# Kernel optimization log

Measured on AMD Instinct MI355X. Metric: run time of the kernel, lower is better.

## Reference

```python
import jax, jax.numpy as jnp
import numpy as np


def setup_inputs() -> dict:
    key = jax.random.key(0)
    k1, k2, k3 = jax.random.split(key, 3)
    B, S, K, N = 4, 2048, 4096, 4096
    x = jax.random.normal(k1, (B, S, K), dtype=jnp.float32)
    # int8 weight table, symmetric range like post-quantization weights
    weight = jax.random.randint(k2, (N, K), -127, 128, dtype=jnp.int32).astype(jnp.int8)
    weight_scale = jnp.float32(0.01)
    bias = jax.random.normal(k3, (N,), dtype=jnp.float32)
    return {"x": x, "weight": weight, "weight_scale": weight_scale, "bias": bias}


def reference(x, weight, weight_scale, bias):
    # dynamic per-tensor activation quantization
    input_scale = jnp.max(jnp.abs(x)) / 127.0
    # torch float->int8 cast truncates toward zero; XLA convert does the same
    x_int8 = jnp.clip(x / input_scale, -127.0, 127.0).astype(jnp.int8)
    orig_shape = x.shape
    # int8 GEMM with int32 accumulation (torch._int_mm equivalent)
    out_int32 = jnp.matmul(
        x_int8.reshape(-1, orig_shape[-1]), weight.T,
        preferred_element_type=jnp.int32,
    )
    out = out_int32.astype(x.dtype) * (input_scale * weight_scale)
    out = out.reshape(*orig_shape[:-1], weight.shape[0])
    out = out + bias
    return out
```

## Files before the change

### kernel.cpp

```cpp
#include <hip/hip_runtime.h>
#include <stdint.h>

static constexpr int KD = 4096;
static constexpr int ND = 4096;

using i32x4 = __attribute__((ext_vector_type(4))) int;

__device__ __forceinline__ void async_copy16(const void* g, void* l) {
    __builtin_amdgcn_global_load_lds(
        (const __attribute__((address_space(1))) void*)g,
        (__attribute__((address_space(3))) void*)l,
        16, 0, 0);
}

__global__ __launch_bounds__(256) void absmax_kernel(
        const float* __restrict__ x, unsigned* __restrict__ out_bits, int n4) {
    int tid = blockIdx.x * blockDim.x + threadIdx.x;
    int stride = gridDim.x * blockDim.x;
    const float4* x4 = (const float4*)x;
    float m = 0.f;
    for (int i = tid; i < n4; i += stride) {
        float4 v = x4[i];
        m = fmaxf(m, fmaxf(fmaxf(fabsf(v.x), fabsf(v.y)),
                           fmaxf(fabsf(v.z), fabsf(v.w))));
    }
    #pragma unroll
    for (int off = 32; off > 0; off >>= 1)
        m = fmaxf(m, __shfl_down(m, off, 64));
    __shared__ float wmax[4];
    int lane = threadIdx.x & 63, w = threadIdx.x >> 6;
    if (lane == 0) wmax[w] = m;
    __syncthreads();
    if (threadIdx.x == 0) {
        float b = fmaxf(fmaxf(wmax[0], wmax[1]), fmaxf(wmax[2], wmax[3]));
        atomicMax(out_bits, __float_as_uint(b));
    }
}

__global__ __launch_bounds__(256) void quant_x_kernel(
        const float* __restrict__ x, const unsigned* __restrict__ mx_bits,
        int8_t* __restrict__ xq) {
    int tid = blockIdx.x * blockDim.x + threadIdx.x;
    float s = __uint_as_float(*mx_bits) * (1.0f / 127.0f);
    const float4* x4 = (const float4*)(x + (size_t)tid * 16);
    int4 packed;
    int* pp = (int*)&packed;
    #pragma unroll
    for (int g = 0; g < 4; ++g) {
        float4 v = x4[g];
        float t0 = fminf(127.f, fmaxf(-127.f, v.x / s));
        float t1 = fminf(127.f, fmaxf(-127.f, v.y / s));
        float t2 = fminf(127.f, fmaxf(-127.f, v.z / s));
        float t3 = fminf(127.f, fmaxf(-127.f, v.w / s));
        int q0 = (int)t0, q1 = (int)t1, q2 = (int)t2, q3 = (int)t3;
        pp[g] = (q0 & 255) | ((q1 & 255) << 8) | ((q2 & 255) << 16) | (q3 << 24);
    }
    ((int4*)xq)[tid] = packed;
}

__global__ __launch_bounds__(256) void pack_w_kernel(
        const int* __restrict__ w, int8_t* __restrict__ wq) {
    int tid = blockIdx.x * blockDim.x + threadIdx.x;
    const int4* w4 = (const int4*)(w + (size_t)tid * 16);
    int4 packed;
    int* pp = (int*)&packed;
    #pragma unroll
    for (int g = 0; g < 4; ++g) {
        int4 v = w4[g];
        pp[g] = (v.x & 255) | ((v.y & 255) << 8) | ((v.z & 255) << 16) | (v.w << 24);
    }
    ((int4*)wq)[tid] = packed;
}

__global__ __launch_bounds__(256) void gemm_i8_kernel(
        const int8_t* __restrict__ Aq,
        const int8_t* __restrict__ Wq,
        const unsigned* __restrict__ mx_bits,
        const float* __restrict__ wscale_p,
        const float* __restrict__ bias,
        float* __restrict__ out) {
    __shared__ __align__(16) int8_t lds_a[128 * 64];
    __shared__ __align__(16) int8_t lds_b[128 * 64];

    const int bx = blockIdx.x;
    const int by = blockIdx.y;
    const int tid  = threadIdx.x;
    const int lane = tid & 63;
    const int w    = tid >> 6;
    const int wm = (w >> 1) * 64;
    const int wn = (w & 1) * 64;
    const int fr = lane & 15;
    const int kc = lane >> 4;

    const int r1 = tid >> 2;
    const int c1 = (tid & 3) ^ ((tid >> 3) & 3);
    const int r2 = r1 + 64;
    const size_t Abase = (size_t)by * 128 * KD;
    const size_t Bbase = (size_t)bx * 128 * KD;
    int8_t* ldsA1 = lds_a + (tid & 192) * 16;
    int8_t* ldsA2 = lds_a + 4096 + (tid & 192) * 16;
    int8_t* ldsB1 = lds_b + (tid & 192) * 16;
    int8_t* ldsB2 = lds_b + 4096 + (tid & 192) * 16;

    i32x4 acc[4][4] = {};

    for (int kt = 0; kt < KD / 64; ++kt) {
        const int k0 = kt * 64;
        async_copy16(Aq + Abase + (size_t)r1 * KD + k0 + c1 * 16, ldsA1);
        async_copy16(Aq + Abase + (size_t)r2 * KD + k0 + c1 * 16, ldsA2);
        async_copy16(Wq + Bbase + (size_t)r1 * KD + k0 + c1 * 16, ldsB1);
        async_copy16(Wq + Bbase + (size_t)r2 * KD + k0 + c1 * 16, ldsB2);
        __syncthreads();

        i32x4 af[4], bf[4];
        #pragma unroll
        for (int i = 0; i < 4; ++i) {
            int row = wm + i * 16 + fr;
            af[i] = *(const i32x4*)(lds_a + row * 64 +
                                    ((kc ^ ((row >> 1) & 3)) << 4));
        }
        #pragma unroll
        for (int j = 0; j < 4; ++j) {
            int row = wn + j * 16 + fr;
            bf[j] = *(const i32x4*)(lds_b + row * 64 +
                                    ((kc ^ ((row >> 1) & 3)) << 4));
        }
        #pragma unroll
        for (int i = 0; i < 4; ++i)
            #pragma unroll
            for (int j = 0; j < 4; ++j)
                acc[i][j] = __builtin_amdgcn_mfma_i32_16x16x64_i8(
                    af[i], bf[j], acc[i][j], 0, 0, 0);
        __syncthreads();
    }

    const float in_scale = __uint_as_float(*mx_bits) * (1.0f / 127.0f);
    const float stot = in_scale * (*wscale_p);
    float bj[4];
    #pragma unroll
    for (int j = 0; j < 4; ++j)
        bj[j] = bias[bx * 128 + wn + j * 16 + fr];

    #pragma unroll
    for (int i = 0; i < 4; ++i) {
        int mrow = by * 128 + wm + i * 16 + kc * 4;
        #pragma unroll
        for (int r = 0; r < 4; ++r) {
            float* orow = out + (size_t)(mrow + r) * ND + bx * 128;
            #pragma unroll
            for (int j = 0; j < 4; ++j)
                orow[wn + j * 16 + fr] = (float)acc[i][j][r] * stot + bj[j];
        }
    }
}

extern "C" void kernel_launch(void* const* d_in, const int* in_sizes, int n_in,
                              void* d_out, int out_size, void* d_ws, size_t ws_size,
                              hipStream_t stream) {
    const float* x      = (const float*)d_in[0];
    const int*   wgt    = (const int*)d_in[1];
    const float* wscale = (const float*)d_in[2];
    const float* bias   = (const float*)d_in[3];
    float* out = (float*)d_out;

    const int M = in_sizes[0] / KD;

    uint8_t* ws = (uint8_t*)d_ws;
    unsigned* mx_bits = (unsigned*)ws;
    int8_t* xq = (int8_t*)(ws + 256);
    int8_t* wq = (int8_t*)(ws + 256 + (size_t)M * KD);

    hipMemsetAsync(mx_bits, 0, 4, stream);
    absmax_kernel<<<1024, 256, 0, stream>>>(x, mx_bits, (M * KD) / 4);
    quant_x_kernel<<<(M * KD / 16) / 256, 256, 0, stream>>>(x, mx_bits, xq);
    pack_w_kernel<<<(ND * KD / 16) / 256, 256, 0, stream>>>(wgt, wq);
    gemm_i8_kernel<<<dim3(ND / 128, M / 128), 256, 0, stream>>>(
        xq, wq, mx_bits, wscale, bias, out);
}
```

Baseline: 451.1 us.

## Switch GEMM to 32x32x32 int8 MFMA and rework preprocessing kernels

The GEMM inner loop now uses 32x32x32 int8 MFMA instructions with 2x2 accumulators per wave instead of 4x4 tiles of 16x16x64, which cuts the instruction count and changes the LDS fragment loads and epilogue layout. The absmax kernel unrolls four independent loads per iteration and launches twice as many blocks. The quantize and pack kernels now handle 4 elements per thread instead of 16, using more threads with narrower stores. The scale is computed by division instead of multiplication by a reciprocal, which may change rounding slightly. The narrower 4-byte stores in the preprocessing kernels could reduce store efficiency.

```diff
diff --git a/kernel.cpp b/kernel.cpp
--- a/kernel.cpp
+++ b/kernel.cpp
@@ -4,7 +4,8 @@
 static constexpr int KD = 4096;
 static constexpr int ND = 4096;
 
-using i32x4 = __attribute__((ext_vector_type(4))) int;
+using i32x4  = __attribute__((ext_vector_type(4)))  int;
+using i32x16 = __attribute__((ext_vector_type(16))) int;
 
 __device__ __forceinline__ void async_copy16(const void* g, void* l) {
     __builtin_amdgcn_global_load_lds(
@@ -18,12 +19,22 @@
     int tid = blockIdx.x * blockDim.x + threadIdx.x;
     int stride = gridDim.x * blockDim.x;
     const float4* x4 = (const float4*)x;
-    float m = 0.f;
-    for (int i = tid; i < n4; i += stride) {
-        float4 v = x4[i];
-        m = fmaxf(m, fmaxf(fmaxf(fabsf(v.x), fabsf(v.y)),
-                           fmaxf(fabsf(v.z), fabsf(v.w))));
+    float m0 = 0.f, m1 = 0.f, m2 = 0.f, m3 = 0.f;
+    for (int i = tid; i < n4; i += 4 * stride) {
+        float4 a = x4[i];
+        float4 b = x4[i + stride];
+        float4 c = x4[i + 2 * stride];
+        float4 d = x4[i + 3 * stride];
+        m0 = fmaxf(m0, fmaxf(fmaxf(fabsf(a.x), fabsf(a.y)),
+                             fmaxf(fabsf(a.z), fabsf(a.w))));
+        m1 = fmaxf(m1, fmaxf(fmaxf(fabsf(b.x), fabsf(b.y)),
+                             fmaxf(fabsf(b.z), fabsf(b.w))));
+        m2 = fmaxf(m2, fmaxf(fmaxf(fabsf(c.x), fabsf(c.y)),
+                             fmaxf(fabsf(c.z), fabsf(c.w))));
+        m3 = fmaxf(m3, fmaxf(fmaxf(fabsf(d.x), fabsf(d.y)),
+                             fmaxf(fabsf(d.z), fabsf(d.w))));
     }
+    float m = fmaxf(fmaxf(m0, m1), fmaxf(m2, m3));
     #pragma unroll
     for (int off = 32; off > 0; off >>= 1)
         m = fmaxf(m, __shfl_down(m, off, 64));
@@ -41,35 +52,21 @@
         const float* __restrict__ x, const unsigned* __restrict__ mx_bits,
         int8_t* __restrict__ xq) {
     int tid = blockIdx.x * blockDim.x + threadIdx.x;
-    float s = __uint_as_float(*mx_bits) * (1.0f / 127.0f);
-    const float4* x4 = (const float4*)(x + (size_t)tid * 16);
-    int4 packed;
-    int* pp = (int*)&packed;
-    #pragma unroll
-    for (int g = 0; g < 4; ++g) {
-        float4 v = x4[g];
-        float t0 = fminf(127.f, fmaxf(-127.f, v.x / s));
-        float t1 = fminf(127.f, fmaxf(-127.f, v.y / s));
-        float t2 = fminf(127.f, fmaxf(-127.f, v.z / s));
-        float t3 = fminf(127.f, fmaxf(-127.f, v.w / s));
-        int q0 = (int)t0, q1 = (int)t1, q2 = (int)t2, q3 = (int)t3;
-        pp[g] = (q0 & 255) | ((q1 & 255) << 8) | ((q2 & 255) << 16) | (q3 << 24);
-    }
-    ((int4*)xq)[tid] = packed;
+    float s = __uint_as_float(*mx_bits) / 127.0f;
+    float4 v = ((const float4*)x)[tid];
+    float t0 = fminf(127.f, fmaxf(-127.f, v.x / s));
+    float t1 = fminf(127.f, fmaxf(-127.f, v.y / s));
+    float t2 = fminf(127.f, fmaxf(-127.f, v.z / s));
+    float t3 = fminf(127.f, fmaxf(-127.f, v.w / s));
+    int q0 = (int)t0, q1 = (int)t1, q2 = (int)t2, q3 = (int)t3;
+    ((int*)xq)[tid] = (q0 & 255) | ((q1 & 255) << 8) | ((q2 & 255) << 16) | (q3 << 24);
 }
 
 __global__ __launch_bounds__(256) void pack_w_kernel(
         const int* __restrict__ w, int8_t* __restrict__ wq) {
     int tid = blockIdx.x * blockDim.x + threadIdx.x;
-    const int4* w4 = (const int4*)(w + (size_t)tid * 16);
-    int4 packed;
-    int* pp = (int*)&packed;
-    #pragma unroll
-    for (int g = 0; g < 4; ++g) {
-        int4 v = w4[g];
-        pp[g] = (v.x & 255) | ((v.y & 255) << 8) | ((v.z & 255) << 16) | (v.w << 24);
-    }
-    ((int4*)wq)[tid] = packed;
+    int4 v = ((const int4*)w)[tid];
+    ((int*)wq)[tid] = (v.x & 255) | ((v.y & 255) << 8) | ((v.z & 255) << 16) | (v.w << 24);
 }
 
 __global__ __launch_bounds__(256) void gemm_i8_kernel(
@@ -89,8 +86,8 @@
     const int w    = tid >> 6;
     const int wm = (w >> 1) * 64;
     const int wn = (w & 1) * 64;
-    const int fr = lane & 15;
-    const int kc = lane >> 4;
+    const int r32 = lane & 31;
+    const int kh  = lane >> 5;
 
     const int r1 = tid >> 2;
     const int c1 = (tid & 3) ^ ((tid >> 3) & 3);
@@ -102,7 +99,7 @@
     int8_t* ldsB1 = lds_b + (tid & 192) * 16;
     int8_t* ldsB2 = lds_b + 4096 + (tid & 192) * 16;
 
-    i32x4 acc[4][4] = {};
+    i32x16 acc[2][2] = {};
 
     for (int kt = 0; kt < KD / 64; ++kt) {
         const int k0 = kt * 64;
@@ -112,44 +109,53 @@
         async_copy16(Wq + Bbase + (size_t)r2 * KD + k0 + c1 * 16, ldsB2);
         __syncthreads();
 
-        i32x4 af[4], bf[4];
+        i32x4 af[2][2], bf[2][2];
         #pragma unroll
-        for (int i = 0; i < 4; ++i) {
-            int row = wm + i * 16 + fr;
-            af[i] = *(const i32x4*)(lds_a + row * 64 +
-                                    ((kc ^ ((row >> 1) & 3)) << 4));
+        for (int i = 0; i < 2; ++i) {
+            int row = wm + i * 32 + r32;
+            int sw = (row >> 1) & 3;
+            #pragma unroll
+            for (int kk = 0; kk < 2; ++kk)
+                af[kk][i] = *(const i32x4*)(lds_a + row * 64 +
+                                            (((kk * 2 + kh) ^ sw) << 4));
         }
         #pragma unroll
-        for (int j = 0; j < 4; ++j) {
-            int row = wn + j * 16 + fr;
-            bf[j] = *(const i32x4*)(lds_b + row * 64 +
-                                    ((kc ^ ((row >> 1) & 3)) << 4));
+        for (int j = 0; j < 2; ++j) {
+            int row = wn + j * 32 + r32;
+            int sw = (row >> 1) & 3;
+            #pragma unroll
+            for (int kk = 0; kk < 2; ++kk)
+                bf[kk][j] = *(const i32x4*)(lds_b + row * 64 +
+                                            (((kk * 2 + kh) ^ sw) << 4));
         }
         #pragma unroll
-        for (int i = 0; i < 4; ++i)
+        for (int kk = 0; kk < 2; ++kk)
             #pragma unroll
-            for (int j = 0; j < 4; ++j)
-                acc[i][j] = __builtin_amdgcn_mfma_i32_16x16x64_i8(
-                    af[i], bf[j], acc[i][j], 0, 0, 0);
+            for (int i = 0; i < 2; ++i)
+                #pragma unroll
+                for (int j = 0; j < 2; ++j)
+                    acc[i][j] = __builtin_amdgcn_mfma_i32_32x32x32_i8(
+                        af[kk][i], bf[kk][j], acc[i][j], 0, 0, 0);
         __syncthreads();
     }
 
-    const float in_scale = __uint_as_float(*mx_bits) * (1.0f / 127.0f);
-    const float stot = in_scale * (*wscale_p);
-    float bj[4];
+    const float stot = (__uint_as_float(*mx_bits) / 127.0f) * (*wscale_p);
+    const int rquad = (lane >> 5) * 4;
+    float bj[2];
     #pragma unroll
-    for (int j = 0; j < 4; ++j)
-        bj[j] = bias[bx * 128 + wn + j * 16 + fr];
+    for (int j = 0; j < 2; ++j)
+        bj[j] = bias[bx * 128 + wn + j * 32 + r32];
 
     #pragma unroll
-    for (int i = 0; i < 4; ++i) {
-        int mrow = by * 128 + wm + i * 16 + kc * 4;
+    for (int i = 0; i < 2; ++i) {
         #pragma unroll
-        for (int r = 0; r < 4; ++r) {
-            float* orow = out + (size_t)(mrow + r) * ND + bx * 128;
+        for (int reg = 0; reg < 16; ++reg) {
+            int row_in = (reg & 3) + 8 * (reg >> 2) + rquad;
+            float* orow = out + (size_t)(by * 128 + wm + i * 32 + row_in) * ND
+                              + bx * 128;
             #pragma unroll
-            for (int j = 0; j < 4; ++j)
-                orow[wn + j * 16 + fr] = (float)acc[i][j][r] * stot + bj[j];
+            for (int j = 0; j < 2; ++j)
+                orow[wn + j * 32 + r32] = (float)acc[i][j][reg] * stot + bj[j];
         }
     }
 }
@@ -171,9 +177,9 @@
     int8_t* wq = (int8_t*)(ws + 256 + (size_t)M * KD);
 
     hipMemsetAsync(mx_bits, 0, 4, stream);
-    absmax_kernel<<<1024, 256, 0, stream>>>(x, mx_bits, (M * KD) / 4);
-    quant_x_kernel<<<(M * KD / 16) / 256, 256, 0, stream>>>(x, mx_bits, xq);
-    pack_w_kernel<<<(ND * KD / 16) / 256, 256, 0, stream>>>(wgt, wq);
+    absmax_kernel<<<2048, 256, 0, stream>>>(x, mx_bits, (M * KD) / 4);
+    quant_x_kernel<<<(M * KD / 4) / 256, 256, 0, stream>>>(x, mx_bits, xq);
+    pack_w_kernel<<<(ND * KD / 4) / 256, 256, 0, stream>>>(wgt, wq);
     gemm_i8_kernel<<<dim3(ND / 128, M / 128), 256, 0, stream>>>(
         xq, wq, mx_bits, wscale, bias, out);
 }
```

Measured after the change: 463.2 us. 2.7% more time.

## Fuse absmax with weight packing, widen GEMM K-tile, simplify quantization

Applied to the files above, without the earlier changes.

Merges the absmax reduction and the int8 weight packing into one prologue launch, with the reduction unrolled four ways for more loads in flight. The GEMM K tile grows from 64 to 128 bytes with an 8-way XOR swizzle, halving the number of barrier-separated iterations and doubling LDS use per block. The quantization kernel now handles one float4 per thread, and the scale is computed with an exact division by 127 to better match the reference. The larger LDS footprint may reduce occupancy, and the prologue's absmax loop assumes the element count divides evenly by four times the stride.

```diff
diff --git a/kernel.cpp b/kernel.cpp
--- a/kernel.cpp
+++ b/kernel.cpp
@@ -3,6 +3,7 @@
 
 static constexpr int KD = 4096;
 static constexpr int ND = 4096;
+static constexpr int BKB = 128;
 
 using i32x4 = __attribute__((ext_vector_type(4))) int;
 
@@ -13,27 +14,54 @@
         16, 0, 0);
 }
 
-__global__ __launch_bounds__(256) void absmax_kernel(
-        const float* __restrict__ x, unsigned* __restrict__ out_bits, int n4) {
-    int tid = blockIdx.x * blockDim.x + threadIdx.x;
-    int stride = gridDim.x * blockDim.x;
-    const float4* x4 = (const float4*)x;
-    float m = 0.f;
-    for (int i = tid; i < n4; i += stride) {
-        float4 v = x4[i];
-        m = fmaxf(m, fmaxf(fmaxf(fabsf(v.x), fabsf(v.y)),
-                           fmaxf(fabsf(v.z), fabsf(v.w))));
-    }
-    #pragma unroll
-    for (int off = 32; off > 0; off >>= 1)
-        m = fmaxf(m, __shfl_down(m, off, 64));
-    __shared__ float wmax[4];
-    int lane = threadIdx.x & 63, w = threadIdx.x >> 6;
-    if (lane == 0) wmax[w] = m;
-    __syncthreads();
-    if (threadIdx.x == 0) {
-        float b = fmaxf(fmaxf(wmax[0], wmax[1]), fmaxf(wmax[2], wmax[3]));
-        atomicMax(out_bits, __float_as_uint(b));
+static constexpr int AB_BLOCKS = 2048;
+
+__global__ __launch_bounds__(256) void prologue_kernel(
+        const float* __restrict__ x, unsigned* __restrict__ out_bits, int n4,
+        const int* __restrict__ w, int8_t* __restrict__ wq) {
+    if (blockIdx.x < AB_BLOCKS) {
+        int tid = blockIdx.x * blockDim.x + threadIdx.x;
+        int stride = AB_BLOCKS * 256;
+        const float4* x4 = (const float4*)x;
+        float m0 = 0.f, m1 = 0.f, m2 = 0.f, m3 = 0.f;
+        for (int i = tid; i < n4; i += 4 * stride) {
+            float4 a = x4[i];
+            float4 b = x4[i + stride];
+            float4 c = x4[i + 2 * stride];
+            float4 d = x4[i + 3 * stride];
+            m0 = fmaxf(m0, fmaxf(fmaxf(fabsf(a.x), fabsf(a.y)),
+                                 fmaxf(fabsf(a.z), fabsf(a.w))));
+            m1 = fmaxf(m1, fmaxf(fmaxf(fabsf(b.x), fabsf(b.y)),
+                                 fmaxf(fabsf(b.z), fabsf(b.w))));
+            m2 = fmaxf(m2, fmaxf(fmaxf(fabsf(c.x), fabsf(c.y)),
+                                 fmaxf(fabsf(c.z), fabsf(c.w))));
+            m3 = fmaxf(m3, fmaxf(fmaxf(fabsf(d.x), fabsf(d.y)),
+                                 fmaxf(fabsf(d.z), fabsf(d.w))));
+        }
+        float m = fmaxf(fmaxf(m0, m1), fmaxf(m2, m3));
+        #pragma unroll
+        for (int off = 32; off > 0; off >>= 1)
+            m = fmaxf(m, __shfl_down(m, off, 64));
+        __shared__ float wmax[4];
+        int lane = threadIdx.x & 63, wv = threadIdx.x >> 6;
+        if (lane == 0) wmax[wv] = m;
+        __syncthreads();
+        if (threadIdx.x == 0) {
+            float b = fmaxf(fmaxf(wmax[0], wmax[1]), fmaxf(wmax[2], wmax[3]));
+            atomicMax(out_bits, __float_as_uint(b));
+        }
+    } else {
+        int t = (blockIdx.x - AB_BLOCKS) * 256 + threadIdx.x;
+        const int4* w4 = (const int4*)(w) + (size_t)t * 4;
+        int4 packed;
+        int* pp = (int*)&packed;
+        #pragma unroll
+        for (int g = 0; g < 4; ++g) {
+            int4 v = w4[g];
+            pp[g] = (v.x & 255) | ((v.y & 255) << 8) |
+                    ((v.z & 255) << 16) | (v.w << 24);
+        }
+        ((int4*)wq)[t] = packed;
     }
 }
 
@@ -41,35 +69,15 @@
         const float* __restrict__ x, const unsigned* __restrict__ mx_bits,
         int8_t* __restrict__ xq) {
     int tid = blockIdx.x * blockDim.x + threadIdx.x;
-    float s = __uint_as_float(*mx_bits) * (1.0f / 127.0f);
-    const float4* x4 = (const float4*)(x + (size_t)tid * 16);
-    int4 packed;
-    int* pp = (int*)&packed;
-    #pragma unroll
-    for (int g = 0; g < 4; ++g) {
-        float4 v = x4[g];
-        float t0 = fminf(127.f, fmaxf(-127.f, v.x / s));
-        float t1 = fminf(127.f, fmaxf(-127.f, v.y / s));
-        float t2 = fminf(127.f, fmaxf(-127.f, v.z / s));
-        float t3 = fminf(127.f, fmaxf(-127.f, v.w / s));
-        int q0 = (int)t0, q1 = (int)t1, q2 = (int)t2, q3 = (int)t3;
-        pp[g] = (q0 & 255) | ((q1 & 255) << 8) | ((q2 & 255) << 16) | (q3 << 24);
-    }
-    ((int4*)xq)[tid] = packed;
-}
-
-__global__ __launch_bounds__(256) void pack_w_kernel(
-        const int* __restrict__ w, int8_t* __restrict__ wq) {
-    int tid = blockIdx.x * blockDim.x + threadIdx.x;
-    const int4* w4 = (const int4*)(w + (size_t)tid * 16);
-    int4 packed;
-    int* pp = (int*)&packed;
-    #pragma unroll
-    for (int g = 0; g < 4; ++g) {
-        int4 v = w4[g];
-        pp[g] = (v.x & 255) | ((v.y & 255) << 8) | ((v.z & 255) << 16) | (v.w << 24);
-    }
-    ((int4*)wq)[tid] = packed;
+    float s = __uint_as_float(*mx_bits) / 127.0f;
+    float4 v = ((const float4*)x)[tid];
+    float t0 = fminf(127.f, fmaxf(-127.f, v.x / s));
+    float t1 = fminf(127.f, fmaxf(-127.f, v.y / s));
+    float t2 = fminf(127.f, fmaxf(-127.f, v.z / s));
+    float t3 = fminf(127.f, fmaxf(-127.f, v.w / s));
+    int q0 = (int)t0, q1 = (int)t1, q2 = (int)t2, q3 = (int)t3;
+    ((int*)xq)[tid] = (q0 & 255) | ((q1 & 255) << 8) |
+                      ((q2 & 255) << 16) | (q3 << 24);
 }
 
 __global__ __launch_bounds__(256) void gemm_i8_kernel(
@@ -79,8 +87,8 @@
         const float* __restrict__ wscale_p,
         const float* __restrict__ bias,
         float* __restrict__ out) {
-    __shared__ __align__(16) int8_t lds_a[128 * 64];
-    __shared__ __align__(16) int8_t lds_b[128 * 64];
+    __shared__ __align__(16) int8_t lds_a[128 * BKB];
+    __shared__ __align__(16) int8_t lds_b[128 * BKB];
 
     const int bx = blockIdx.x;
     const int by = blockIdx.y;
@@ -92,50 +100,51 @@
     const int fr = lane & 15;
     const int kc = lane >> 4;
 
-    const int r1 = tid >> 2;
-    const int c1 = (tid & 3) ^ ((tid >> 3) & 3);
-    const int r2 = r1 + 64;
-    const size_t Abase = (size_t)by * 128 * KD;
-    const size_t Bbase = (size_t)bx * 128 * KD;
-    int8_t* ldsA1 = lds_a + (tid & 192) * 16;
-    int8_t* ldsA2 = lds_a + 4096 + (tid & 192) * 16;
-    int8_t* ldsB1 = lds_b + (tid & 192) * 16;
-    int8_t* ldsB2 = lds_b + 4096 + (tid & 192) * 16;
+    const int rr  = tid >> 3;
+    const int gch = (tid & 7) ^ ((tid >> 3) & 7);
+    const size_t Abase = (size_t)by * 128 * KD + (size_t)rr * KD + gch * 16;
+    const size_t Bbase = (size_t)bx * 128 * KD + (size_t)rr * KD + gch * 16;
+    const int ldsoff = (tid & 192) * 16;
 
     i32x4 acc[4][4] = {};
 
-    for (int kt = 0; kt < KD / 64; ++kt) {
-        const int k0 = kt * 64;
-        async_copy16(Aq + Abase + (size_t)r1 * KD + k0 + c1 * 16, ldsA1);
-        async_copy16(Aq + Abase + (size_t)r2 * KD + k0 + c1 * 16, ldsA2);
-        async_copy16(Wq + Bbase + (size_t)r1 * KD + k0 + c1 * 16, ldsB1);
-        async_copy16(Wq + Bbase + (size_t)r2 * KD + k0 + c1 * 16, ldsB2);
+    for (int kt = 0; kt < KD / BKB; ++kt) {
+        const int kb = kt * BKB;
+        #pragma unroll
+        for (int c = 0; c < 4; ++c) {
+            async_copy16(Aq + Abase + (size_t)(c * 32) * KD + kb,
+                         lds_a + c * 4096 + ldsoff);
+            async_copy16(Wq + Bbase + (size_t)(c * 32) * KD + kb,
+                         lds_b + c * 4096 + ldsoff);
+        }
         __syncthreads();
 
-        i32x4 af[4], bf[4];
         #pragma unroll
-        for (int i = 0; i < 4; ++i) {
-            int row = wm + i * 16 + fr;
-            af[i] = *(const i32x4*)(lds_a + row * 64 +
-                                    ((kc ^ ((row >> 1) & 3)) << 4));
+        for (int s = 0; s < 2; ++s) {
+            i32x4 af[4], bf[4];
+            #pragma unroll
+            for (int i = 0; i < 4; ++i) {
+                int row = wm + i * 16 + fr;
+                int lc = (s * 4 + kc) ^ (row & 7);
+                af[i] = *(const i32x4*)(lds_a + row * BKB + lc * 16);
+            }
+            #pragma unroll
+            for (int j = 0; j < 4; ++j) {
+                int row = wn + j * 16 + fr;
+                int lc = (s * 4 + kc) ^ (row & 7);
+                bf[j] = *(const i32x4*)(lds_b + row * BKB + lc * 16);
+            }
+            #pragma unroll
+            for (int i = 0; i < 4; ++i)
+                #pragma unroll
+                for (int j = 0; j < 4; ++j)
+                    acc[i][j] = __builtin_amdgcn_mfma_i32_16x16x64_i8(
+                        af[i], bf[j], acc[i][j], 0, 0, 0);
         }
-        #pragma unroll
-        for (int j = 0; j < 4; ++j) {
-            int row = wn + j * 16 + fr;
-            bf[j] = *(const i32x4*)(lds_b + row * 64 +
-                                    ((kc ^ ((row >> 1) & 3)) << 4));
-        }
-        #pragma unroll
-        for (int i = 0; i < 4; ++i)
-            #pragma unroll
-            for (int j = 0; j < 4; ++j)
-                acc[i][j] = __builtin_amdgcn_mfma_i32_16x16x64_i8(
-                    af[i], bf[j], acc[i][j], 0, 0, 0);
         __syncthreads();
     }
 
-    const float in_scale = __uint_as_float(*mx_bits) * (1.0f / 127.0f);
-    const float stot = in_scale * (*wscale_p);
+    const float stot = (__uint_as_float(*mx_bits) / 127.0f) * (*wscale_p);
     float bj[4];
     #pragma unroll
     for (int j = 0; j < 4; ++j)
@@ -170,10 +179,11 @@
     int8_t* xq = (int8_t*)(ws + 256);
     int8_t* wq = (int8_t*)(ws + 256 + (size_t)M * KD);
 
+    const int pk_blocks = (ND * KD / 16) / 256;
     hipMemsetAsync(mx_bits, 0, 4, stream);
-    absmax_kernel<<<1024, 256, 0, stream>>>(x, mx_bits, (M * KD) / 4);
-    quant_x_kernel<<<(M * KD / 16) / 256, 256, 0, stream>>>(x, mx_bits, xq);
-    pack_w_kernel<<<(ND * KD / 16) / 256, 256, 0, stream>>>(wgt, wq);
+    prologue_kernel<<<AB_BLOCKS + pk_blocks, 256, 0, stream>>>(
+        x, mx_bits, (M * KD) / 4, wgt, wq);
+    quant_x_kernel<<<(M * KD / 4) / 256, 256, 0, stream>>>(x, mx_bits, xq);
     gemm_i8_kernel<<<dim3(ND / 128, M / 128), 256, 0, stream>>>(
         xq, wq, mx_bits, wscale, bias, out);
 }
```

Result: faster. 426.7 us (-5.4%).
